# Performance work log

Hardware: AMD Instinct MI355X
Metric: run time of the kernel (lower is better)

The kernel has to match this reference:

```python
import jax, jax.numpy as jnp
import numpy as np

B, NL, NP = 8, 256, 16384
DL, DP = 10, 4          # ligand / protein atom-type vocab sizes (one-hot prefix)
L_BIND, L_MREG = 1.0, 0.1
DELTA, EPS, A_C, B_C = 0.01, 1.0, 1.0, 1.0
BOX = 30.0              # Angstrom box for coordinates


def setup_inputs() -> dict:
    key = jax.random.key(0)
    ks = jax.random.split(key, 10)
    return {
        "predicted_noise": jax.random.normal(ks[0], (B, NL, 3), jnp.float32),
        "target_coords": jax.random.normal(ks[1], (B, NL, 3), jnp.float32),
        "scaffold_coords": jax.random.normal(ks[2], (B, NL, 3), jnp.float32),
        "target_coords2": jax.random.uniform(ks[3], (B, NL, 3), jnp.float32) * BOX,
        "target_features": jax.random.uniform(ks[4], (B, NL, DL), jnp.float32),
        "mask": jax.random.uniform(ks[5], (B, NL), jnp.float32),
        "protein_coords": jax.random.uniform(ks[6], (B, NP, 3), jnp.float32) * BOX,
        "protein_features": jax.random.uniform(ks[7], (B, NP, DP), jnp.float32),
        "lig_charge_table": jax.random.normal(ks[8], (DL,), jnp.float32) * 0.3,
        "prot_charge_table": jax.random.normal(ks[9], (DP,), jnp.float32) * 0.3,
    }


def _cdist(x, p):
    # x: [B, NL, 3], p: [B, NP, 3] -> [B, NL, NP] Euclidean distances
    x2 = jnp.sum(x * x, axis=-1)
    p2 = jnp.sum(p * p, axis=-1)
    d2 = x2[:, :, None] + p2[:, None, :] - 2.0 * jnp.einsum('bnd,bmd->bnm', x, p)
    return jnp.sqrt(jnp.maximum(d2, 0.0))


def _binding_energy(x0, prot, lig_feat, prot_feat, lig_tab, prot_tab):
    # atom charges from one-hot prefix of features (argmax lookup)
    ql = lig_tab[jnp.argmax(lig_feat[..., :DL], axis=-1)]    # [B, NL]
    qp = prot_tab[jnp.argmax(prot_feat[..., :DP], axis=-1)]  # [B, NP]
    d = _cdist(x0, prot) + DELTA                             # [B, NL, NP]
    inv = 1.0 / d
    inv6 = inv ** 6
    elec = jnp.sum(ql[:, :, None] * qp[:, None, :] * inv / EPS, axis=(1, 2))
    vdw = jnp.sum(A_C * inv6 * inv6 - B_C * inv6, axis=(1, 2))
    return elec + vdw  # [B]


def reference(predicted_noise, target_coords, scaffold_coords, target_coords2,
              target_features, mask, protein_coords, protein_features,
              lig_charge_table, prot_charge_table):
    msum = jnp.sum(mask)
    # masked denoising MSE
    mse = (predicted_noise - target_coords) ** 2
    loss_denoise = jnp.sum(mse * mask[..., None]) / msum
    # protein-guided binding energy, mean over batch
    loss_bind = jnp.mean(_binding_energy(target_coords2, protein_coords,
                                         target_features, protein_features,
                                         lig_charge_table, prot_charge_table))
    # mask regularization
    mask_diff = jnp.sum((scaffold_coords - target_coords) ** 2, axis=-1)
    loss_mreg = jnp.sum(mask_diff * mask) / msum
    return loss_denoise + L_BIND * loss_bind + L_MREG * loss_mreg
```

## Files before the change

kernel.cpp:

```cpp
#include <hip/hip_runtime.h>
#include <math.h>

#define B   8
#define NL  256
#define NP  16384
#define DL  10
#define DP  4

#define DELTA  0.01f

#define NBINDBLK 1024
#define NMSE     8
#define LATOMS   128

typedef float v4f __attribute__((ext_vector_type(4)));

static __device__ __forceinline__ float fast_sqrtf(float x) {
#if __has_builtin(__builtin_amdgcn_sqrtf)
    return __builtin_amdgcn_sqrtf(x);
#else
    return sqrtf(x);
#endif
}
static __device__ __forceinline__ float fast_rcpf(float x) {
#if __has_builtin(__builtin_amdgcn_rcpf)
    return __builtin_amdgcn_rcpf(x);
#else
    return 1.0f / x;
#endif
}

__global__ __launch_bounds__(256) void pair_mse_kernel(
    const float* __restrict__ prot_coords,
    const float* __restrict__ prot_feat,
    const float* __restrict__ tc2,
    const float* __restrict__ lig_feat,
    const float* __restrict__ lig_tab,
    const float* __restrict__ prot_tab,
    const float* __restrict__ pred_noise,
    const float* __restrict__ tgt_coords,
    const float* __restrict__ scaf_coords,
    const float* __restrict__ mask,
    double*      __restrict__ partials)
{
    const int tid  = threadIdx.x;
    const int blk  = blockIdx.x;
    const int lane = tid & 63, w = tid >> 6;

    __shared__ double sred[4][3];

    if (blk < NBINDBLK) {
        const int lhalf  = blk & 1;
        const int pchunk = (blk >> 1) & 63;
        const int b      = blk >> 7;

        __shared__ __align__(16) float sx[LATOMS], sy[LATOMS], sz[LATOMS], sw[LATOMS];
        __shared__ float sc[LATOMS * 3];
        __shared__ float sfeat[LATOMS * DL];

        const int abase = b * NL + lhalf * LATOMS;

        {
            const float* csrc = tc2 + (size_t)abase * 3;
            #pragma unroll
            for (int t = tid; t < LATOMS * 3; t += 256) sc[t] = csrc[t];
            const float* fsrc = lig_feat + (size_t)abase * DL;
            #pragma unroll
            for (int t = tid; t < LATOMS * DL; t += 256) sfeat[t] = fsrc[t];
        }

        const int m = b * NP + pchunk * 256 + tid;
        const float* pc = prot_coords + (size_t)m * 3;
        const float px = pc[0], py = pc[1], pz = pc[2];
        const float4 pf = reinterpret_cast<const float4*>(prot_feat)[m];
        float qb = pf.x, qp = prot_tab[0];
        { float t = prot_tab[1]; if (pf.y > qb) { qb = pf.y; qp = t; } }
        { float t = prot_tab[2]; if (pf.z > qb) { qb = pf.z; qp = t; } }
        { float t = prot_tab[3]; if (pf.w > qb) { qb = pf.w; qp = t; } }

        __syncthreads();

        if (tid < LATOMS) {
            float best = sfeat[tid * DL];
            float q = lig_tab[0];
            #pragma unroll
            for (int j = 1; j < DL; ++j) {
                float v = sfeat[tid * DL + j];
                float t = lig_tab[j];
                if (v > best) { best = v; q = t; }
            }
            sx[tid] = sc[tid * 3 + 0];
            sy[tid] = sc[tid * 3 + 1];
            sz[tid] = sc[tid * 3 + 2];
            sw[tid] = q;
        }
        __syncthreads();

        v4f eacc = {0.f, 0.f, 0.f, 0.f}, vacc = {0.f, 0.f, 0.f, 0.f};
        #pragma unroll 4
        for (int j = 0; j < LATOMS; j += 4) {
            v4f lx = *(const v4f*)&sx[j];
            v4f ly = *(const v4f*)&sy[j];
            v4f lz = *(const v4f*)&sz[j];
            v4f lw = *(const v4f*)&sw[j];
            v4f dx = lx - px;
            v4f dy = ly - py;
            v4f dz = lz - pz;
            v4f d2 = __builtin_elementwise_fma(dx, dx,
                     __builtin_elementwise_fma(dy, dy, dz * dz));
            v4f d;
            d.x = fast_sqrtf(d2.x); d.y = fast_sqrtf(d2.y);
            d.z = fast_sqrtf(d2.z); d.w = fast_sqrtf(d2.w);
            d += DELTA;
            v4f inv;
            inv.x = fast_rcpf(d.x); inv.y = fast_rcpf(d.y);
            inv.z = fast_rcpf(d.z); inv.w = fast_rcpf(d.w);
            v4f inv2 = inv * inv;
            v4f inv6 = inv2 * inv2 * inv2;
            eacc = __builtin_elementwise_fma(lw, inv, eacc);
            vacc = __builtin_elementwise_fma(inv6, inv6 - 1.0f, vacc);
        }

        double e = (double)(qp * ((eacc.x + eacc.y) + (eacc.z + eacc.w)));
        double v = (double)((vacc.x + vacc.y) + (vacc.z + vacc.w));
        #pragma unroll
        for (int off = 32; off > 0; off >>= 1) {
            e += __shfl_down(e, off, 64);
            v += __shfl_down(v, off, 64);
        }
        if (lane == 0) { sred[w][0] = e; sred[w][1] = v; }
        __syncthreads();
        if (tid == 0) {
            partials[2 * blk]     = sred[0][0] + sred[1][0] + sred[2][0] + sred[3][0];
            partials[2 * blk + 1] = sred[0][1] + sred[1][1] + sred[2][1] + sred[3][1];
        }
    } else {
        const int idx = blk - NBINDBLK;
        const int i   = idx * 256 + tid;
        float mk = mask[i];
        float a0 = pred_noise[3*i+0] - tgt_coords[3*i+0];
        float a1 = pred_noise[3*i+1] - tgt_coords[3*i+1];
        float a2 = pred_noise[3*i+2] - tgt_coords[3*i+2];
        double de = (double)mk * ((double)a0*a0 + (double)a1*a1 + (double)a2*a2);
        float s0 = scaf_coords[3*i+0] - tgt_coords[3*i+0];
        float s1 = scaf_coords[3*i+1] - tgt_coords[3*i+1];
        float s2 = scaf_coords[3*i+2] - tgt_coords[3*i+2];
        double mr = (double)mk * ((double)s0*s0 + (double)s1*s1 + (double)s2*s2);
        double ms = (double)mk;
        #pragma unroll
        for (int off = 32; off > 0; off >>= 1) {
            de += __shfl_down(de, off, 64);
            mr += __shfl_down(mr, off, 64);
            ms += __shfl_down(ms, off, 64);
        }
        if (lane == 0) { sred[w][0] = de; sred[w][1] = mr; sred[w][2] = ms; }
        __syncthreads();
        if (tid == 0) {
            partials[2*NBINDBLK + idx*3 + 0] = sred[0][0]+sred[1][0]+sred[2][0]+sred[3][0];
            partials[2*NBINDBLK + idx*3 + 1] = sred[0][1]+sred[1][1]+sred[2][1]+sred[3][1];
            partials[2*NBINDBLK + idx*3 + 2] = sred[0][2]+sred[1][2]+sred[2][2]+sred[3][2];
        }
    }
}

__global__ __launch_bounds__(256) void finalize_kernel(
    const double* __restrict__ partials,
    float* __restrict__ out)
{
    const int tid = threadIdx.x;
    const int lane = tid & 63, w = tid >> 6;
    double el = 0.0, vd = 0.0;
    for (int i = tid; i < NBINDBLK; i += 256) {
        el += partials[2*i];
        vd += partials[2*i + 1];
    }
    double de = 0.0, mr = 0.0, ms = 0.0;
    if (tid < NMSE) {
        de = partials[2*NBINDBLK + tid*3 + 0];
        mr = partials[2*NBINDBLK + tid*3 + 1];
        ms = partials[2*NBINDBLK + tid*3 + 2];
    }
    #pragma unroll
    for (int off = 32; off > 0; off >>= 1) {
        el += __shfl_down(el, off, 64);
        vd += __shfl_down(vd, off, 64);
        de += __shfl_down(de, off, 64);
        mr += __shfl_down(mr, off, 64);
        ms += __shfl_down(ms, off, 64);
    }
    __shared__ double s[4][5];
    if (lane == 0) { s[w][0]=el; s[w][1]=vd; s[w][2]=de; s[w][3]=mr; s[w][4]=ms; }
    __syncthreads();
    if (tid == 0) {
        el = s[0][0]+s[1][0]+s[2][0]+s[3][0];
        vd = s[0][1]+s[1][1]+s[2][1]+s[3][1];
        de = s[0][2]+s[1][2]+s[2][2]+s[3][2];
        mr = s[0][3]+s[1][3]+s[2][3]+s[3][3];
        ms = s[0][4]+s[1][4]+s[2][4]+s[3][4];
        double loss_bind = (el + vd) / (double)B;
        double loss = de / ms + loss_bind + 0.1 * (mr / ms);
        out[0] = (float)loss;
    }
}

extern "C" void kernel_launch(void* const* d_in, const int* in_sizes, int n_in,
                              void* d_out, int out_size, void* d_ws, size_t ws_size,
                              hipStream_t stream)
{
    const float* pred_noise  = (const float*)d_in[0];
    const float* tgt_coords  = (const float*)d_in[1];
    const float* scaf_coords = (const float*)d_in[2];
    const float* tc2         = (const float*)d_in[3];
    const float* lig_feat    = (const float*)d_in[4];
    const float* mask        = (const float*)d_in[5];
    const float* prot_coords = (const float*)d_in[6];
    const float* prot_feat   = (const float*)d_in[7];
    const float* lig_tab     = (const float*)d_in[8];
    const float* prot_tab    = (const float*)d_in[9];
    float* out = (float*)d_out;

    double* partials = (double*)d_ws;

    pair_mse_kernel<<<NBINDBLK + NMSE, 256, 0, stream>>>(
        prot_coords, prot_feat, tc2, lig_feat, lig_tab, prot_tab,
        pred_noise, tgt_coords, scaf_coords, mask, partials);
    finalize_kernel<<<1, 256, 0, stream>>>(partials, out);
}
```

Measured before the change: 91.41 us.

## Register-block 4 protein atoms per thread and fuse finalize via atomic last-block

Each thread now handles four protein atoms against 32 ligand atoms, reusing each LDS ligand load across four pairs. The block grid is re-split so each block covers 1024 protein atoms and one eighth of the ligand atoms. The separate finalize kernel is replaced by double atomics plus a completion counter, and the last block computes the loss. This adds a memset launch and atomic contention on five addresses. Float-atomic ordering also makes the summation order nondeterministic.

```diff
diff --git a/kernel.cpp b/kernel.cpp
--- a/kernel.cpp
+++ b/kernel.cpp
@@ -11,7 +11,9 @@
 
 #define NBINDBLK 1024
 #define NMSE     8
-#define LATOMS   128
+#define NBLK     (NBINDBLK + NMSE)
+#define LATOMS   32
+#define PBLK     4
 
 typedef float v4f __attribute__((ext_vector_type(4)));
 
@@ -30,7 +32,11 @@
 #endif
 }
 
-__global__ __launch_bounds__(256) void pair_mse_kernel(
+static __device__ __forceinline__ void atomic_add_f64(double* p, double v) {
+    unsafeAtomicAdd(p, v);
+}
+
+__global__ __launch_bounds__(256, 4) void fused_kernel(
     const float* __restrict__ prot_coords,
     const float* __restrict__ prot_feat,
     const float* __restrict__ tc2,
@@ -41,7 +47,9 @@
     const float* __restrict__ tgt_coords,
     const float* __restrict__ scaf_coords,
     const float* __restrict__ mask,
-    double*      __restrict__ partials)
+    double*      __restrict__ acc,
+    unsigned*    __restrict__ counter,
+    float*       __restrict__ out)
 {
     const int tid  = threadIdx.x;
     const int blk  = blockIdx.x;
@@ -50,33 +58,38 @@
     __shared__ double sred[4][3];
 
     if (blk < NBINDBLK) {
-        const int lhalf  = blk & 1;
-        const int pchunk = (blk >> 1) & 63;
-        const int b      = blk >> 7;
+        const int leighth = blk & 7;
+        const int pchunk  = (blk >> 3) & 15;
+        const int b       = blk >> 7;
 
         __shared__ __align__(16) float sx[LATOMS], sy[LATOMS], sz[LATOMS], sw[LATOMS];
         __shared__ float sc[LATOMS * 3];
         __shared__ float sfeat[LATOMS * DL];
 
-        const int abase = b * NL + lhalf * LATOMS;
+        const int abase = b * NL + leighth * LATOMS;
 
         {
             const float* csrc = tc2 + (size_t)abase * 3;
-            #pragma unroll
-            for (int t = tid; t < LATOMS * 3; t += 256) sc[t] = csrc[t];
+            if (tid < LATOMS * 3) sc[tid] = csrc[tid];
             const float* fsrc = lig_feat + (size_t)abase * DL;
             #pragma unroll
             for (int t = tid; t < LATOMS * DL; t += 256) sfeat[t] = fsrc[t];
         }
 
-        const int m = b * NP + pchunk * 256 + tid;
-        const float* pc = prot_coords + (size_t)m * 3;
-        const float px = pc[0], py = pc[1], pz = pc[2];
-        const float4 pf = reinterpret_cast<const float4*>(prot_feat)[m];
-        float qb = pf.x, qp = prot_tab[0];
-        { float t = prot_tab[1]; if (pf.y > qb) { qb = pf.y; qp = t; } }
-        { float t = prot_tab[2]; if (pf.z > qb) { qb = pf.z; qp = t; } }
-        { float t = prot_tab[3]; if (pf.w > qb) { qb = pf.w; qp = t; } }
+        const int mbase = b * NP + pchunk * 1024 + tid;
+        float px[PBLK], py[PBLK], pz[PBLK], qp[PBLK];
+        #pragma unroll
+        for (int k = 0; k < PBLK; ++k) {
+            const int m = mbase + k * 256;
+            const float* pc = prot_coords + (size_t)m * 3;
+            px[k] = pc[0]; py[k] = pc[1]; pz[k] = pc[2];
+            const float4 pf = reinterpret_cast<const float4*>(prot_feat)[m];
+            float qb = pf.x; float q = prot_tab[0];
+            { float t = prot_tab[1]; if (pf.y > qb) { qb = pf.y; q = t; } }
+            { float t = prot_tab[2]; if (pf.z > qb) { qb = pf.z; q = t; } }
+            { float t = prot_tab[3]; if (pf.w > qb) { qb = pf.w; q = t; } }
+            qp[k] = q;
+        }
 
         __syncthreads();
 
@@ -96,33 +109,44 @@
         }
         __syncthreads();
 
-        v4f eacc = {0.f, 0.f, 0.f, 0.f}, vacc = {0.f, 0.f, 0.f, 0.f};
-        #pragma unroll 4
+        v4f eacc[PBLK], vacc[PBLK];
+        #pragma unroll
+        for (int k = 0; k < PBLK; ++k) {
+            eacc[k] = (v4f){0.f,0.f,0.f,0.f};
+            vacc[k] = (v4f){0.f,0.f,0.f,0.f};
+        }
+
+        #pragma unroll 2
         for (int j = 0; j < LATOMS; j += 4) {
             v4f lx = *(const v4f*)&sx[j];
             v4f ly = *(const v4f*)&sy[j];
             v4f lz = *(const v4f*)&sz[j];
             v4f lw = *(const v4f*)&sw[j];
-            v4f dx = lx - px;
-            v4f dy = ly - py;
-            v4f dz = lz - pz;
-            v4f d2 = __builtin_elementwise_fma(dx, dx,
-                     __builtin_elementwise_fma(dy, dy, dz * dz));
-            v4f d;
-            d.x = fast_sqrtf(d2.x); d.y = fast_sqrtf(d2.y);
-            d.z = fast_sqrtf(d2.z); d.w = fast_sqrtf(d2.w);
-            d += DELTA;
-            v4f inv;
-            inv.x = fast_rcpf(d.x); inv.y = fast_rcpf(d.y);
-            inv.z = fast_rcpf(d.z); inv.w = fast_rcpf(d.w);
-            v4f inv2 = inv * inv;
-            v4f inv6 = inv2 * inv2 * inv2;
-            eacc = __builtin_elementwise_fma(lw, inv, eacc);
-            vacc = __builtin_elementwise_fma(inv6, inv6 - 1.0f, vacc);
-        }
-
-        double e = (double)(qp * ((eacc.x + eacc.y) + (eacc.z + eacc.w)));
-        double v = (double)((vacc.x + vacc.y) + (vacc.z + vacc.w));
+            #pragma unroll
+            for (int k = 0; k < PBLK; ++k) {
+                v4f dx = lx - px[k], dy = ly - py[k], dz = lz - pz[k];
+                v4f d2 = __builtin_elementwise_fma(dx, dx,
+                         __builtin_elementwise_fma(dy, dy, dz * dz));
+                v4f d;
+                d.x = fast_sqrtf(d2.x); d.y = fast_sqrtf(d2.y);
+                d.z = fast_sqrtf(d2.z); d.w = fast_sqrtf(d2.w);
+                d += DELTA;
+                v4f inv;
+                inv.x = fast_rcpf(d.x); inv.y = fast_rcpf(d.y);
+                inv.z = fast_rcpf(d.z); inv.w = fast_rcpf(d.w);
+                v4f inv2 = inv * inv;
+                v4f inv6 = inv2 * inv2 * inv2;
+                eacc[k] = __builtin_elementwise_fma(lw, inv, eacc[k]);
+                vacc[k] = __builtin_elementwise_fma(inv6, inv6 - 1.0f, vacc[k]);
+            }
+        }
+
+        double e = 0.0, v = 0.0;
+        #pragma unroll
+        for (int k = 0; k < PBLK; ++k) {
+            e += (double)(qp[k] * ((eacc[k].x + eacc[k].y) + (eacc[k].z + eacc[k].w)));
+            v += (double)((vacc[k].x + vacc[k].y) + (vacc[k].z + vacc[k].w));
+        }
         #pragma unroll
         for (int off = 32; off > 0; off >>= 1) {
             e += __shfl_down(e, off, 64);
@@ -131,8 +155,8 @@
         if (lane == 0) { sred[w][0] = e; sred[w][1] = v; }
         __syncthreads();
         if (tid == 0) {
-            partials[2 * blk]     = sred[0][0] + sred[1][0] + sred[2][0] + sred[3][0];
-            partials[2 * blk + 1] = sred[0][1] + sred[1][1] + sred[2][1] + sred[3][1];
+            atomic_add_f64(&acc[0], sred[0][0] + sred[1][0] + sred[2][0] + sred[3][0]);
+            atomic_add_f64(&acc[1], sred[0][1] + sred[1][1] + sred[2][1] + sred[3][1]);
         }
     } else {
         const int idx = blk - NBINDBLK;
@@ -156,47 +180,25 @@
         if (lane == 0) { sred[w][0] = de; sred[w][1] = mr; sred[w][2] = ms; }
         __syncthreads();
         if (tid == 0) {
-            partials[2*NBINDBLK + idx*3 + 0] = sred[0][0]+sred[1][0]+sred[2][0]+sred[3][0];
-            partials[2*NBINDBLK + idx*3 + 1] = sred[0][1]+sred[1][1]+sred[2][1]+sred[3][1];
-            partials[2*NBINDBLK + idx*3 + 2] = sred[0][2]+sred[1][2]+sred[2][2]+sred[3][2];
+            atomic_add_f64(&acc[2], sred[0][0]+sred[1][0]+sred[2][0]+sred[3][0]);
+            atomic_add_f64(&acc[3], sred[0][1]+sred[1][1]+sred[2][1]+sred[3][1]);
+            atomic_add_f64(&acc[4], sred[0][2]+sred[1][2]+sred[2][2]+sred[3][2]);
         }
     }
-}
-
-__global__ __launch_bounds__(256) void finalize_kernel(
-    const double* __restrict__ partials,
-    float* __restrict__ out)
-{
-    const int tid = threadIdx.x;
-    const int lane = tid & 63, w = tid >> 6;
-    double el = 0.0, vd = 0.0;
-    for (int i = tid; i < NBINDBLK; i += 256) {
-        el += partials[2*i];
-        vd += partials[2*i + 1];
+
+    __shared__ unsigned sOld;
+    if (tid == 0) {
+        asm volatile("s_waitcnt vmcnt(0)" ::: "memory");
+        sOld = __hip_atomic_fetch_add(counter, 1u, __ATOMIC_RELAXED,
+                                      __HIP_MEMORY_SCOPE_AGENT);
     }
-    double de = 0.0, mr = 0.0, ms = 0.0;
-    if (tid < NMSE) {
-        de = partials[2*NBINDBLK + tid*3 + 0];
-        mr = partials[2*NBINDBLK + tid*3 + 1];
-        ms = partials[2*NBINDBLK + tid*3 + 2];
-    }
-    #pragma unroll
-    for (int off = 32; off > 0; off >>= 1) {
-        el += __shfl_down(el, off, 64);
-        vd += __shfl_down(vd, off, 64);
-        de += __shfl_down(de, off, 64);
-        mr += __shfl_down(mr, off, 64);
-        ms += __shfl_down(ms, off, 64);
-    }
-    __shared__ double s[4][5];
-    if (lane == 0) { s[w][0]=el; s[w][1]=vd; s[w][2]=de; s[w][3]=mr; s[w][4]=ms; }
     __syncthreads();
-    if (tid == 0) {
-        el = s[0][0]+s[1][0]+s[2][0]+s[3][0];
-        vd = s[0][1]+s[1][1]+s[2][1]+s[3][1];
-        de = s[0][2]+s[1][2]+s[2][2]+s[3][2];
-        mr = s[0][3]+s[1][3]+s[2][3]+s[3][3];
-        ms = s[0][4]+s[1][4]+s[2][4]+s[3][4];
+    if (sOld == NBLK - 1 && tid == 0) {
+        double el = __hip_atomic_load(&acc[0], __ATOMIC_RELAXED, __HIP_MEMORY_SCOPE_AGENT);
+        double vd = __hip_atomic_load(&acc[1], __ATOMIC_RELAXED, __HIP_MEMORY_SCOPE_AGENT);
+        double de = __hip_atomic_load(&acc[2], __ATOMIC_RELAXED, __HIP_MEMORY_SCOPE_AGENT);
+        double mr = __hip_atomic_load(&acc[3], __ATOMIC_RELAXED, __HIP_MEMORY_SCOPE_AGENT);
+        double ms = __hip_atomic_load(&acc[4], __ATOMIC_RELAXED, __HIP_MEMORY_SCOPE_AGENT);
         double loss_bind = (el + vd) / (double)B;
         double loss = de / ms + loss_bind + 0.1 * (mr / ms);
         out[0] = (float)loss;
@@ -219,10 +221,11 @@
     const float* prot_tab    = (const float*)d_in[9];
     float* out = (float*)d_out;
 
-    double* partials = (double*)d_ws;
-
-    pair_mse_kernel<<<NBINDBLK + NMSE, 256, 0, stream>>>(
+    double*   acc     = (double*)d_ws;
+    unsigned* counter = (unsigned*)((char*)d_ws + 48);
+
+    hipMemsetAsync(d_ws, 0, 64, stream);
+    fused_kernel<<<NBLK, 256, 0, stream>>>(
         prot_coords, prot_feat, tc2, lig_feat, lig_tab, prot_tab,
-        pred_noise, tgt_coords, scaf_coords, mask, partials);
-    finalize_kernel<<<1, 256, 0, stream>>>(partials, out);
-}
+        pred_noise, tgt_coords, scaf_coords, mask, acc, counter, out);
+}
```

After: 120.7 us. +32.1%, slower.

## Register-block four protein atoms per thread with smaller ligand tiles

Applied to the files above, without the earlier changes.

Each thread now handles four protein atoms held in registers, and each block stages 32 ligand atoms instead of 128. This keeps the grid at 1024 binding blocks, but each LDS ligand load is now reused across four protein atoms, which cuts shared-memory traffic per pair. Launch bounds now request 4 blocks per CU. The extra accumulators raise register pressure, and the smaller ligand tile means more per-block setup relative to the pair work.

```diff
diff --git a/kernel.cpp b/kernel.cpp
--- a/kernel.cpp
+++ b/kernel.cpp
@@ -11,7 +11,8 @@
 
 #define NBINDBLK 1024
 #define NMSE     8
-#define LATOMS   128
+#define LATOMS   32
+#define PBLK     4
 
 typedef float v4f __attribute__((ext_vector_type(4)));
 
@@ -30,7 +31,7 @@
 #endif
 }
 
-__global__ __launch_bounds__(256) void pair_mse_kernel(
+__global__ __launch_bounds__(256, 4) void pair_mse_kernel(
     const float* __restrict__ prot_coords,
     const float* __restrict__ prot_feat,
     const float* __restrict__ tc2,
@@ -50,33 +51,38 @@
     __shared__ double sred[4][3];
 
     if (blk < NBINDBLK) {
-        const int lhalf  = blk & 1;
-        const int pchunk = (blk >> 1) & 63;
-        const int b      = blk >> 7;
+        const int leighth = blk & 7;
+        const int pchunk  = (blk >> 3) & 15;
+        const int b       = blk >> 7;
 
         __shared__ __align__(16) float sx[LATOMS], sy[LATOMS], sz[LATOMS], sw[LATOMS];
         __shared__ float sc[LATOMS * 3];
         __shared__ float sfeat[LATOMS * DL];
 
-        const int abase = b * NL + lhalf * LATOMS;
+        const int abase = b * NL + leighth * LATOMS;
 
         {
             const float* csrc = tc2 + (size_t)abase * 3;
-            #pragma unroll
-            for (int t = tid; t < LATOMS * 3; t += 256) sc[t] = csrc[t];
+            if (tid < LATOMS * 3) sc[tid] = csrc[tid];
             const float* fsrc = lig_feat + (size_t)abase * DL;
             #pragma unroll
             for (int t = tid; t < LATOMS * DL; t += 256) sfeat[t] = fsrc[t];
         }
 
-        const int m = b * NP + pchunk * 256 + tid;
-        const float* pc = prot_coords + (size_t)m * 3;
-        const float px = pc[0], py = pc[1], pz = pc[2];
-        const float4 pf = reinterpret_cast<const float4*>(prot_feat)[m];
-        float qb = pf.x, qp = prot_tab[0];
-        { float t = prot_tab[1]; if (pf.y > qb) { qb = pf.y; qp = t; } }
-        { float t = prot_tab[2]; if (pf.z > qb) { qb = pf.z; qp = t; } }
-        { float t = prot_tab[3]; if (pf.w > qb) { qb = pf.w; qp = t; } }
+        const int mbase = b * NP + pchunk * 1024 + tid;
+        float px[PBLK], py[PBLK], pz[PBLK], qp[PBLK];
+        #pragma unroll
+        for (int k = 0; k < PBLK; ++k) {
+            const int m = mbase + k * 256;
+            const float* pc = prot_coords + (size_t)m * 3;
+            px[k] = pc[0]; py[k] = pc[1]; pz[k] = pc[2];
+            const float4 pf = reinterpret_cast<const float4*>(prot_feat)[m];
+            float qb = pf.x; float q = prot_tab[0];
+            { float t = prot_tab[1]; if (pf.y > qb) { qb = pf.y; q = t; } }
+            { float t = prot_tab[2]; if (pf.z > qb) { qb = pf.z; q = t; } }
+            { float t = prot_tab[3]; if (pf.w > qb) { qb = pf.w; q = t; } }
+            qp[k] = q;
+        }
 
         __syncthreads();
 
@@ -96,33 +102,44 @@
         }
         __syncthreads();
 
-        v4f eacc = {0.f, 0.f, 0.f, 0.f}, vacc = {0.f, 0.f, 0.f, 0.f};
-        #pragma unroll 4
+        v4f eacc[PBLK], vacc[PBLK];
+        #pragma unroll
+        for (int k = 0; k < PBLK; ++k) {
+            eacc[k] = (v4f){0.f,0.f,0.f,0.f};
+            vacc[k] = (v4f){0.f,0.f,0.f,0.f};
+        }
+
+        #pragma unroll 2
         for (int j = 0; j < LATOMS; j += 4) {
             v4f lx = *(const v4f*)&sx[j];
             v4f ly = *(const v4f*)&sy[j];
             v4f lz = *(const v4f*)&sz[j];
             v4f lw = *(const v4f*)&sw[j];
-            v4f dx = lx - px;
-            v4f dy = ly - py;
-            v4f dz = lz - pz;
-            v4f d2 = __builtin_elementwise_fma(dx, dx,
-                     __builtin_elementwise_fma(dy, dy, dz * dz));
-            v4f d;
-            d.x = fast_sqrtf(d2.x); d.y = fast_sqrtf(d2.y);
-            d.z = fast_sqrtf(d2.z); d.w = fast_sqrtf(d2.w);
-            d += DELTA;
-            v4f inv;
-            inv.x = fast_rcpf(d.x); inv.y = fast_rcpf(d.y);
-            inv.z = fast_rcpf(d.z); inv.w = fast_rcpf(d.w);
-            v4f inv2 = inv * inv;
-            v4f inv6 = inv2 * inv2 * inv2;
-            eacc = __builtin_elementwise_fma(lw, inv, eacc);
-            vacc = __builtin_elementwise_fma(inv6, inv6 - 1.0f, vacc);
-        }
-
-        double e = (double)(qp * ((eacc.x + eacc.y) + (eacc.z + eacc.w)));
-        double v = (double)((vacc.x + vacc.y) + (vacc.z + vacc.w));
+            #pragma unroll
+            for (int k = 0; k < PBLK; ++k) {
+                v4f dx = lx - px[k], dy = ly - py[k], dz = lz - pz[k];
+                v4f d2 = __builtin_elementwise_fma(dx, dx,
+                         __builtin_elementwise_fma(dy, dy, dz * dz));
+                v4f d;
+                d.x = fast_sqrtf(d2.x); d.y = fast_sqrtf(d2.y);
+                d.z = fast_sqrtf(d2.z); d.w = fast_sqrtf(d2.w);
+                d += DELTA;
+                v4f inv;
+                inv.x = fast_rcpf(d.x); inv.y = fast_rcpf(d.y);
+                inv.z = fast_rcpf(d.z); inv.w = fast_rcpf(d.w);
+                v4f inv2 = inv * inv;
+                v4f inv6 = inv2 * inv2 * inv2;
+                eacc[k] = __builtin_elementwise_fma(lw, inv, eacc[k]);
+                vacc[k] = __builtin_elementwise_fma(inv6, inv6 - 1.0f, vacc[k]);
+            }
+        }
+
+        double e = 0.0, v = 0.0;
+        #pragma unroll
+        for (int k = 0; k < PBLK; ++k) {
+            e += (double)(qp[k] * ((eacc[k].x + eacc[k].y) + (eacc[k].z + eacc[k].w)));
+            v += (double)((vacc[k].x + vacc[k].y) + (vacc[k].z + vacc[k].w));
+        }
         #pragma unroll
         for (int off = 32; off > 0; off >>= 1) {
             e += __shfl_down(e, off, 64);
```

Result: slower. 94.47 us (+3.3%).
